# Optimization experiments

Measured on AMD Instinct MI355X. Metric: run time of the kernel, lower is better.

Reference implementation:

```python
import jax, jax.numpy as jnp
import numpy as np

B, N, DIN, A = 64, 64, 64, 32
DOUT = 128          # obs_output_dim == obs_act_output_dim == 128 (required by module wiring)
OA_IN = DIN + A     # obs_act_input_dim = 96


def _w(key, shape):
    fan_in = shape[-1]
    return jax.random.normal(key, shape, jnp.float32) / jnp.sqrt(jnp.float32(fan_in))


def setup_inputs() -> dict:
    key = jax.random.key(0)
    ks = jax.random.split(key, 14)
    return {
        "states": jax.random.normal(ks[0], (B, N, DIN), jnp.float32),
        "policies": jax.random.uniform(ks[1], (B, N, A), jnp.float32),
        "actions": jax.random.uniform(ks[2], (B, N, A), jnp.float32),
        # state_embed_preproc: Linear(obs_input_dim, 128) + LeakyReLU
        "W_se_pre": _w(ks[3], (128, DIN)),
        "b_se_pre": jnp.zeros((128,), jnp.float32),
        # key/query layers (shared between both attention stages in forward)
        "W_key": _w(ks[4], (DOUT, 128)),
        "W_query": _w(ks[5], (DOUT, 128)),
        # state_embed: Linear(obs_output_dim, 128) + LeakyReLU
        "W_se": _w(ks[6], (128, DOUT)),
        "b_se": jnp.zeros((128,), jnp.float32),
        # state_act_pol_embed: Linear(obs_act_input_dim, 128) + LeakyReLU
        "W_sap": _w(ks[7], (128, OA_IN)),
        "b_sap": jnp.zeros((128,), jnp.float32),
        # attention_value_layer: Linear(128, obs_act_output_dim)
        "W_av": _w(ks[8], (DOUT, 128)),
        # final value head
        "W_f1": _w(ks[9], (64, DOUT)),
        "W_f2": _w(ks[10], (1, 64)),
    }


def reference(states, policies, actions, W_se_pre, b_se_pre, W_key, W_query,
              W_se, b_se, W_sap, b_sap, W_av, W_f1, W_f2):
    lrelu = jax.nn.leaky_relu  # negative_slope=0.01, matches torch default
    d_k = W_key.shape[0]
    inv_sqrt_dk = 1.0 / jnp.sqrt(jnp.asarray(d_k, states.dtype))

    # stage 1: self-attention over agents on raw-state embeddings
    e = lrelu(states @ W_se_pre.T + b_se_pre)                       # [B,N,128]
    q1 = e @ W_query.T
    k1 = e @ W_key.T
    w_pre = jax.nn.softmax(jnp.einsum('bid,bjd->bij', q1, k1) * inv_sqrt_dk, axis=-1)
    # NB: attention_value_layer_preproc output is overwritten in the original forward;
    # the effective value is weight_preproc @ states_embed_preproc.
    av_pre = jnp.einsum('bij,bjd->bid', w_pre, e)                   # [B,N,128]

    # stage 2: self-attention weights over agents on re-embedded states
    se = lrelu(av_pre @ W_se.T + b_se)                              # [B,N,128]
    q2 = se @ W_query.T
    k2 = se @ W_key.T
    w = jax.nn.softmax(jnp.einsum('bid,bjd->bij', q2, k2) * inv_sqrt_dk, axis=-1)

    # obs_actions_policies[b,j,k] = (state_k, policy_k) if j==k else (state_k, action_k)
    obs_act = jnp.concatenate([states, actions], axis=-1)           # [B,N,OA_IN]
    obs_pol = jnp.concatenate([states, policies], axis=-1)
    n = states.shape[1]
    eye = jnp.eye(n, dtype=states.dtype)[None, :, :, None]          # [1,N,N,1]
    oap = eye * obs_pol[:, None, :, :] + (1.0 - eye) * obs_act[:, None, :, :]  # [B,N,N,OA_IN]

    emb = lrelu(oap @ W_sap.T + b_sap)                              # [B,N,N,128]
    av = emb @ W_av.T                                               # [B,N,N,DOUT]

    # fused form of repeat->weight->sum: node[b,i,j,d] = sum_k w[b,i,k] * av[b,j,k,d]
    node = jnp.einsum('bik,bjkd->bijd', w, av)                      # [B,N,N,DOUT]

    value = lrelu(node @ W_f1.T) @ W_f2.T                           # [B,N,N,1]
    return value, w_pre, w
```

## Files before the change

### kernel.cpp

```cpp
#include <hip/hip_runtime.h>

#define DEVFN __device__ __forceinline__

constexpr int BNN = 64 * 64 * 64;
constexpr float SCALE = 0.08838834764831845f;
constexpr float NSLOPE = 0.01f;

constexpr int OFF_WPRET = 0;
constexpr int OFF_WQT   = 8192;
constexpr int OFF_M     = 24576;
constexpr int OFF_WSET  = 40960;
constexpr int OFF_WSAPT = 57344;
constexpr int OFF_WAVT  = 69632;
constexpr int OFF_WF1T  = 86016;
constexpr int OFF_E     = 98304;
constexpr int OFF_Q     = 622592;
constexpr int OFF_ET    = 1146880;
constexpr int OFF_SET   = 1671168;
constexpr int OFF_AVACT = 2195456;
constexpr int OFF_HD    = 2719744;


DEVFN void st128(int tid, const float* __restrict__ src, float* __restrict__ Bs, int rows) {
  const int n4 = rows * 32;
  for (int idx = tid; idx < n4; idx += 512) {
    const int r = idx >> 5, c = idx & 31;
    *reinterpret_cast<float4*>(&Bs[r * 132 + c * 4]) =
        *reinterpret_cast<const float4*>(&src[r * 128 + c * 4]);
  }
}

DEVFN void st64x(int tid, const float* __restrict__ src, float* __restrict__ Bs) {
  for (int idx = tid; idx < 1024; idx += 512) {
    const int r = idx >> 4, c = idx & 15;
    *reinterpret_cast<float4*>(&Bs[r * 68 + c * 4]) =
        *reinterpret_cast<const float4*>(&src[r * 64 + c * 4]);
  }
}

DEVFN void wrT(int tid, const float* __restrict__ S, float* __restrict__ dst, int rq) {
  const int fr = tid >> 2, a4 = tid & 3;
  float t[4];
#pragma unroll
  for (int i = 0; i < 4; ++i) t[i] = S[(a4 * 4 + i) * 132 + fr];
  float4 v; v.x = t[0]; v.y = t[1]; v.z = t[2]; v.w = t[3];
  *reinterpret_cast<float4*>(&dst[fr * 64 + rq * 16 + a4 * 4]) = v;
}


DEVFN void g1(int tid, const float* __restrict__ A, int lda,
              const float* __restrict__ Bs, int K, float (&acc)[4]) {
  const int c0 = (tid & 31) * 4, rg = tid >> 5;
#pragma unroll 8
  for (int k = 0; k < K; ++k) {
    const float4 bv = *reinterpret_cast<const float4*>(&Bs[k * 132 + c0]);
    const float a = A[rg * lda + k];
    acc[0] += a * bv.x; acc[1] += a * bv.y; acc[2] += a * bv.z; acc[3] += a * bv.w;
  }
}

DEVFN void g2A(int tid, const float* __restrict__ A0, const float* __restrict__ A1,
               int lda, const float* __restrict__ Bs, int K,
               float (&a0)[4], float (&a1)[4]) {
  const int c0 = (tid & 31) * 4, rg = tid >> 5;
#pragma unroll 4
  for (int k = 0; k < K; ++k) {
    const float4 bv = *reinterpret_cast<const float4*>(&Bs[k * 132 + c0]);
    const float x = A0[rg * lda + k];
    const float y = A1[rg * lda + k];
    a0[0] += x * bv.x; a0[1] += x * bv.y; a0[2] += x * bv.z; a0[3] += x * bv.w;
    a1[0] += y * bv.x; a1[1] += y * bv.y; a1[2] += y * bv.z; a1[3] += y * bv.w;
  }
}

DEVFN void gH(int tid, const float* __restrict__ A, int lda,
              const float* __restrict__ Bs, int K, float (&acc)[2]) {
  const int c0 = (tid & 31) * 2, rg = tid >> 5;
#pragma unroll 8
  for (int k = 0; k < K; ++k) {
    const float2 bv = *reinterpret_cast<const float2*>(&Bs[k * 68 + c0]);
    const float a = A[rg * lda + k];
    acc[0] += a * bv.x; acc[1] += a * bv.y;
  }
}

template<bool ACT, bool HASB>
DEVFN void epi(int tid, const float (&acc)[4], float* __restrict__ O, int ldo,
               const float* __restrict__ bias) {
  const int c0 = (tid & 31) * 4, rg = tid >> 5;
  float t[4];
#pragma unroll
  for (int i = 0; i < 4; ++i) {
    float x = acc[i];
    if constexpr (HASB) x += bias[c0 + i];
    if constexpr (ACT) x = (x > 0.f) ? x : NSLOPE * x;
    t[i] = x;
  }
  float4 v; v.x = t[0]; v.y = t[1]; v.z = t[2]; v.w = t[3];
  *reinterpret_cast<float4*>(&O[rg * ldo + c0]) = v;
}


DEVFN void score_half(int tid, const float* __restrict__ Qs, int hoff,
                      const float* __restrict__ Ks, float (&acc)[2]) {
  const int j = tid & 63, iw = tid >> 6;
#pragma unroll 2
  for (int kt = 0; kt < 64; kt += 8) {
    float qv[2][8];
#pragma unroll
    for (int r = 0; r < 2; ++r) {
      *reinterpret_cast<float4*>(&qv[r][0]) =
          *reinterpret_cast<const float4*>(&Qs[(iw * 2 + r) * 132 + hoff + kt]);
      *reinterpret_cast<float4*>(&qv[r][4]) =
          *reinterpret_cast<const float4*>(&Qs[(iw * 2 + r) * 132 + hoff + kt + 4]);
    }
#pragma unroll
    for (int kk = 0; kk < 8; ++kk) {
      const float kv = Ks[(kt + kk) * 68 + j];
      acc[0] += qv[0][kk] * kv;
      acc[1] += qv[1][kk] * kv;
    }
  }
}

DEVFN void softmax_write(int tid, float (&acc)[2], float* __restrict__ Wp,
                         float* __restrict__ gout) {
  const int j = tid & 63, iw = tid >> 6;
#pragma unroll
  for (int r = 0; r < 2; ++r) {
    float v = acc[r] * SCALE;
    float m = v;
#pragma unroll
    for (int off = 32; off > 0; off >>= 1) m = fmaxf(m, __shfl_xor(m, off, 64));
    const float p = __expf(v - m);
    float s = p;
#pragma unroll
    for (int off = 32; off > 0; off >>= 1) s += __shfl_xor(s, off, 64);
    const float w = p / s;
    Wp[(iw * 2 + r) * 68 + j] = w;
    gout[(iw * 2 + r) * 64 + j] = w;
  }
}


__global__ void transpose_all(const float* __restrict__ Wpre, const float* __restrict__ Wq,
                              const float* __restrict__ Wse, const float* __restrict__ Wsap,
                              const float* __restrict__ Wav, const float* __restrict__ Wf1,
                              float* __restrict__ ws) {
  const int m = blockIdx.y;
  const float* src; int Cout, K, off;
  switch (m) {
    case 0: src = Wpre; Cout = 128; K = 64;  off = OFF_WPRET; break;
    case 1: src = Wq;   Cout = 128; K = 128; off = OFF_WQT;   break;
    case 2: src = Wse;  Cout = 128; K = 128; off = OFF_WSET;  break;
    case 3: src = Wsap; Cout = 128; K = 96;  off = OFF_WSAPT; break;
    case 4: src = Wav;  Cout = 128; K = 128; off = OFF_WAVT;  break;
    default: src = Wf1; Cout = 64;  K = 128; off = OFF_WF1T;  break;
  }
  const int idx = blockIdx.x * 256 + threadIdx.x;
  if (idx < Cout * K) {
    const int c = idx / K, k = idx - c * K;
    ws[off + k * Cout + c] = src[idx];
  }
}

__global__ __launch_bounds__(512) void make_M(const float* __restrict__ Wkey,
                                              float* __restrict__ ws) {
  __shared__ float As[16 * 132];
  __shared__ float Bs[64 * 132];
  const int tid = threadIdx.x;
  const int r0 = blockIdx.x * 16;
  {
    const int r = tid >> 5, c = tid & 31;
    *reinterpret_cast<float4*>(&As[r * 132 + c * 4]) =
        *reinterpret_cast<const float4*>(&ws[OFF_WQT + (r0 + r) * 128 + c * 4]);
  }
  const int c0 = (tid & 31) * 4, rg = tid >> 5;
  float acc[4] = {};
  for (int h = 0; h < 2; ++h) {
    __syncthreads();
    st128(tid, Wkey + h * 8192, Bs, 64);
    __syncthreads();
#pragma unroll 8
    for (int k = 0; k < 64; ++k) {
      const float4 bv = *reinterpret_cast<const float4*>(&Bs[k * 132 + c0]);
      const float a = As[rg * 132 + h * 64 + k];
      acc[0] += a * bv.x; acc[1] += a * bv.y; acc[2] += a * bv.z; acc[3] += a * bv.w;
    }
  }
  float4 v; v.x = acc[0]; v.y = acc[1]; v.z = acc[2]; v.w = acc[3];
  *reinterpret_cast<float4*>(&ws[OFF_M + (r0 + rg) * 128 + c0]) = v;
}

__global__ __launch_bounds__(512) void P1(const float* __restrict__ states,
                                          const float* __restrict__ policies,
                                          const float* __restrict__ actions,
                                          const float* __restrict__ b_sap,
                                          const float* __restrict__ b_se_pre,
                                          float* __restrict__ ws) {
  __shared__ float Xa[16 * 100], Xp[16 * 100];
  __shared__ float Ea[16 * 132], Ep[16 * 132], Dd[16 * 132], Er[16 * 132];
  __shared__ float Bs[64 * 132];
  const int tid = threadIdx.x;
  const int wid = ((blockIdx.x & 7) << 5) | (blockIdx.x >> 3);
  const int b = wid >> 2, rq = wid & 3;
  const int r0g = b * 64 + rq * 16;

  for (int idx = tid; idx < 1024; idx += 512) {
    const int r = idx >> 6, c = idx & 63;
    const float s = states[(r0g + r) * 64 + c];
    Xa[r * 100 + c] = s;
    Xp[r * 100 + c] = s;
  }
  {
    const int r = tid >> 5, c = tid & 31;
    Xa[r * 100 + 64 + c] = actions[(r0g + r) * 32 + c];
    Xp[r * 100 + 64 + c] = policies[(r0g + r) * 32 + c];
  }
  st128(tid, ws + OFF_WSAPT, Bs, 64);
  __syncthreads();
  float aa[4] = {}, ap[4] = {};
  g2A(tid, Xa, Xp, 100, Bs, 64, aa, ap);
  __syncthreads();
  st128(tid, ws + OFF_WSAPT + 8192, Bs, 32);
  __syncthreads();
  g2A(tid, Xa + 64, Xp + 64, 100, Bs, 32, aa, ap);
  epi<true, true>(tid, aa, Ea, 132, b_sap);
  epi<true, true>(tid, ap, Ep, 132, b_sap);
  __syncthreads();
  for (int idx = tid; idx < 2048; idx += 512) {
    const int r = idx >> 7, c = idx & 127;
    Ep[r * 132 + c] -= Ea[r * 132 + c];
  }
  __syncthreads();
  st128(tid, ws + OFF_WAVT, Bs, 64);
  __syncthreads();
  float av[4] = {}, dl[4] = {};
  g2A(tid, Ea, Ep, 132, Bs, 64, av, dl);
  __syncthreads();
  st128(tid, ws + OFF_WAVT + 8192, Bs, 64);
  __syncthreads();
  g2A(tid, Ea + 64, Ep + 64, 132, Bs, 64, av, dl);
  epi<false, false>(tid, av, ws + OFF_AVACT + r0g * 128, 128, nullptr);
  epi<false, false>(tid, dl, Dd, 132, nullptr);
  __syncthreads();
  st64x(tid, ws + OFF_WF1T, Bs);
  __syncthreads();
  float ah[2] = {};
  gH(tid, Dd, 132, Bs, 64, ah);
  __syncthreads();
  st64x(tid, ws + OFF_WF1T + 4096, Bs);
  __syncthreads();
  gH(tid, Dd + 64, 132, Bs, 64, ah);
  {
    const int c0 = (tid & 31) * 2, rg = tid >> 5;
    float2 v; v.x = ah[0]; v.y = ah[1];
    *reinterpret_cast<float2*>(&ws[OFF_HD + (r0g + rg) * 64 + c0]) = v;
  }
  __syncthreads();
  st128(tid, ws + OFF_WPRET, Bs, 64);
  __syncthreads();
  {
    float ae[4] = {};
    g1(tid, Xa, 100, Bs, 64, ae);
    const int c0 = (tid & 31) * 4, rg = tid >> 5;
    float t[4];
#pragma unroll
    for (int i = 0; i < 4; ++i) {
      float x = ae[i] + b_se_pre[c0 + i];
      t[i] = (x > 0.f) ? x : NSLOPE * x;
    }
    float4 v; v.x = t[0]; v.y = t[1]; v.z = t[2]; v.w = t[3];
    *reinterpret_cast<float4*>(&Er[rg * 132 + c0]) = v;
    *reinterpret_cast<float4*>(&ws[OFF_E + (r0g + rg) * 128 + c0]) = v;
  }
  __syncthreads();
  wrT(tid, Er, ws + OFF_ET + b * 8192, rq);
  st128(tid, ws + OFF_M, Bs, 64);
  __syncthreads();
  float af[4] = {};
  g1(tid, Er, 132, Bs, 64, af);
  __syncthreads();
  st128(tid, ws + OFF_M + 8192, Bs, 64);
  __syncthreads();
  g1(tid, Er + 64, 132, Bs, 64, af);
  epi<false, false>(tid, af, ws + OFF_Q + r0g * 128, 128, nullptr);
}

__global__ __launch_bounds__(512) void P3(const float* __restrict__ b_se,
                                          float* __restrict__ ws,
                                          float* __restrict__ out) {
  __shared__ float Qs[16 * 132];
  __shared__ float Bs[64 * 132];
  __shared__ float Wp[16 * 68], AV[16 * 132], SEr[16 * 132];
  const int tid = threadIdx.x;
  const int wid = ((blockIdx.x & 7) << 5) | (blockIdx.x >> 3);
  const int b = wid >> 2, rq = wid & 3;
  const int r0g = b * 64 + rq * 16;

  {
    const int r = tid >> 5, c = tid & 31;
    *reinterpret_cast<float4*>(&Qs[r * 132 + c * 4]) =
        *reinterpret_cast<const float4*>(&ws[OFF_Q + (r0g + r) * 128 + c * 4]);
  }
  st64x(tid, ws + OFF_ET + b * 8192, Bs);
  __syncthreads();
  float sc[2] = {};
  score_half(tid, Qs, 0, Bs, sc);
  __syncthreads();
  st64x(tid, ws + OFF_ET + b * 8192 + 4096, Bs);
  __syncthreads();
  score_half(tid, Qs, 64, Bs, sc);
  softmax_write(tid, sc, Wp, out + BNN + b * 4096 + rq * 1024);
  __syncthreads();
  st128(tid, ws + OFF_E + b * 8192, Bs, 64);
  __syncthreads();
  {
    float a[4] = {};
    g1(tid, Wp, 68, Bs, 64, a);
    epi<false, false>(tid, a, AV, 132, nullptr);
  }
  __syncthreads();
  st128(tid, ws + OFF_WSET, Bs, 64);
  __syncthreads();
  float as[4] = {};
  g1(tid, AV, 132, Bs, 64, as);
  __syncthreads();
  st128(tid, ws + OFF_WSET + 8192, Bs, 64);
  __syncthreads();
  g1(tid, AV + 64, 132, Bs, 64, as);
  {
    const int c0 = (tid & 31) * 4, rg = tid >> 5;
    float t[4];
#pragma unroll
    for (int i = 0; i < 4; ++i) {
      float x = as[i] + b_se[c0 + i];
      t[i] = (x > 0.f) ? x : NSLOPE * x;
    }
    float4 v; v.x = t[0]; v.y = t[1]; v.z = t[2]; v.w = t[3];
    *reinterpret_cast<float4*>(&SEr[rg * 132 + c0]) = v;
  }
  __syncthreads();
  wrT(tid, SEr, ws + OFF_SET + b * 8192, rq);
  st128(tid, ws + OFF_M, Bs, 64);
  __syncthreads();
  float af[4] = {};
  g1(tid, SEr, 132, Bs, 64, af);
  __syncthreads();
  st128(tid, ws + OFF_M + 8192, Bs, 64);
  __syncthreads();
  g1(tid, SEr + 64, 132, Bs, 64, af);
  epi<false, false>(tid, af, ws + OFF_Q + r0g * 128, 128, nullptr);
}

__global__ __launch_bounds__(512) void P4(const float* __restrict__ Wf2g,
                                          float* __restrict__ ws,
                                          float* __restrict__ out) {
  __shared__ float Qs[16 * 132];
  __shared__ float Bs[64 * 132];
  __shared__ float Wp[16 * 68], NB[16 * 132], Hb[16 * 66];
  __shared__ float Hd[64 * 69];
  __shared__ float Wf2s[64];
  const int tid = threadIdx.x;
  const int wid = ((blockIdx.x & 7) << 5) | (blockIdx.x >> 3);
  const int b = wid >> 2, rq = wid & 3;
  const int r0g = b * 64 + rq * 16;

  for (int idx = tid; idx < 4096; idx += 512)
    Hd[(idx >> 6) * 69 + (idx & 63)] = ws[OFF_HD + b * 4096 + idx];
  if (tid < 64) Wf2s[tid] = Wf2g[tid];
  {
    const int r = tid >> 5, c = tid & 31;
    *reinterpret_cast<float4*>(&Qs[r * 132 + c * 4]) =
        *reinterpret_cast<const float4*>(&ws[OFF_Q + (r0g + r) * 128 + c * 4]);
  }
  st64x(tid, ws + OFF_SET + b * 8192, Bs);
  __syncthreads();
  float sc[2] = {};
  score_half(tid, Qs, 0, Bs, sc);
  __syncthreads();
  st64x(tid, ws + OFF_SET + b * 8192 + 4096, Bs);
  __syncthreads();
  score_half(tid, Qs, 64, Bs, sc);
  softmax_write(tid, sc, Wp, out + 2 * BNN + b * 4096 + rq * 1024);
  __syncthreads();
  st128(tid, ws + OFF_AVACT + b * 8192, Bs, 64);
  __syncthreads();
  {
    float a[4] = {};
    g1(tid, Wp, 68, Bs, 64, a);
    epi<false, false>(tid, a, NB, 132, nullptr);
  }
  __syncthreads();
  st64x(tid, ws + OFF_WF1T, Bs);
  __syncthreads();
  float ah[2] = {};
  gH(tid, NB, 132, Bs, 64, ah);
  __syncthreads();
  st64x(tid, ws + OFF_WF1T + 4096, Bs);
  __syncthreads();
  gH(tid, NB + 64, 132, Bs, 64, ah);
  {
    const int c0 = (tid & 31) * 2, rg = tid >> 5;
    float2 v; v.x = ah[0]; v.y = ah[1];
    *reinterpret_cast<float2*>(&Hb[rg * 66 + c0]) = v;
  }
  __syncthreads();
  const int j = tid & 63, iw = tid >> 6;
  float wv[2], a2[2] = {0.f, 0.f};
#pragma unroll
  for (int r = 0; r < 2; ++r) wv[r] = Wp[(iw * 2 + r) * 68 + j];
  for (int f = 0; f < 64; ++f) {
    const float hdv = Hd[j * 69 + f];
    const float wf = Wf2s[f];
#pragma unroll
    for (int r = 0; r < 2; ++r) {
      float t = Hb[(iw * 2 + r) * 66 + f] + wv[r] * hdv;
      t = (t > 0.f) ? t : NSLOPE * t;
      a2[r] += t * wf;
    }
  }
#pragma unroll
  for (int r = 0; r < 2; ++r)
    out[(r0g + iw * 2 + r) * 64 + j] = a2[r];
}

extern "C" void kernel_launch(void* const* d_in, const int* in_sizes, int n_in,
                              void* d_out, int out_size, void* d_ws, size_t ws_size,
                              hipStream_t stream) {
  const float* states   = (const float*)d_in[0];
  const float* policies = (const float*)d_in[1];
  const float* actions  = (const float*)d_in[2];
  const float* W_se_pre = (const float*)d_in[3];
  const float* b_se_pre = (const float*)d_in[4];
  const float* W_key    = (const float*)d_in[5];
  const float* W_query  = (const float*)d_in[6];
  const float* W_se     = (const float*)d_in[7];
  const float* b_se     = (const float*)d_in[8];
  const float* W_sap    = (const float*)d_in[9];
  const float* b_sap    = (const float*)d_in[10];
  const float* W_av     = (const float*)d_in[11];
  const float* W_f1     = (const float*)d_in[12];
  const float* W_f2     = (const float*)d_in[13];
  float* out = (float*)d_out;
  float* ws  = (float*)d_ws;

  transpose_all<<<dim3(64, 6), dim3(256), 0, stream>>>(
      W_se_pre, W_query, W_se, W_sap, W_av, W_f1, ws);
  make_M<<<dim3(8), dim3(512), 0, stream>>>(W_key, ws);
  P1<<<dim3(256), dim3(512), 0, stream>>>(states, policies, actions, b_sap, b_se_pre, ws);
  P3<<<dim3(256), dim3(512), 0, stream>>>(b_se, ws, out);
  P4<<<dim3(256), dim3(512), 0, stream>>>(W_f2, ws, out);
}
```

Before: 68.45 us.

## Precompute av_act·Wf1 in P1 and share state projection across act/pol

P1 now computes the state part of the state-action-policy embedding once and adds separate action and policy contributions, instead of running the full 96-wide GEMM twice. It also multiplies the action-value rows by Wf1 up front, storing a 64-wide HA buffer in place of the 128-wide av_act. P4 can then apply the attention weights directly to HA (using linearity: (W·AV)·Wf1 = W·(AV·Wf1)), dropping a 64x128x64 GEMM and one set of Wf1 staging loads. This cuts P4 work and workspace traffic at the cost of a little extra GEMM work and one extra barrier in P1.

```diff
diff --git a/kernel.cpp b/kernel.cpp
--- a/kernel.cpp
+++ b/kernel.cpp
@@ -17,7 +17,7 @@
 constexpr int OFF_Q     = 622592;
 constexpr int OFF_ET    = 1146880;
 constexpr int OFF_SET   = 1671168;
-constexpr int OFF_AVACT = 2195456;
+constexpr int OFF_HA    = 2195456;
 constexpr int OFF_HD    = 2719744;
 
 
@@ -81,6 +81,20 @@
     const float2 bv = *reinterpret_cast<const float2*>(&Bs[k * 68 + c0]);
     const float a = A[rg * lda + k];
     acc[0] += a * bv.x; acc[1] += a * bv.y;
+  }
+}
+
+DEVFN void gH2(int tid, const float* __restrict__ A0, const float* __restrict__ A1,
+               int lda, const float* __restrict__ Bs, int K,
+               float (&a0)[2], float (&a1)[2]) {
+  const int c0 = (tid & 31) * 2, rg = tid >> 5;
+#pragma unroll 4
+  for (int k = 0; k < K; ++k) {
+    const float2 bv = *reinterpret_cast<const float2*>(&Bs[k * 68 + c0]);
+    const float x = A0[rg * lda + k];
+    const float y = A1[rg * lda + k];
+    a0[0] += x * bv.x; a0[1] += x * bv.y;
+    a1[0] += y * bv.x; a1[1] += y * bv.y;
   }
 }
 
@@ -198,8 +212,10 @@
                                           const float* __restrict__ b_sap,
                                           const float* __restrict__ b_se_pre,
                                           float* __restrict__ ws) {
-  __shared__ float Xa[16 * 100], Xp[16 * 100];
-  __shared__ float Ea[16 * 132], Ep[16 * 132], Dd[16 * 132], Er[16 * 132];
+  __shared__ float S[16 * 68];
+  __shared__ float Aa[16 * 36], Ap[16 * 36];
+  __shared__ float Ea[16 * 132];
+  __shared__ float Ep[16 * 132], Dd[16 * 132], Er[16 * 132];
   __shared__ float Bs[64 * 132];
   const int tid = threadIdx.x;
   const int wid = ((blockIdx.x & 7) << 5) | (blockIdx.x >> 3);
@@ -208,23 +224,23 @@
 
   for (int idx = tid; idx < 1024; idx += 512) {
     const int r = idx >> 6, c = idx & 63;
-    const float s = states[(r0g + r) * 64 + c];
-    Xa[r * 100 + c] = s;
-    Xp[r * 100 + c] = s;
+    S[r * 68 + c] = states[(r0g + r) * 64 + c];
   }
   {
     const int r = tid >> 5, c = tid & 31;
-    Xa[r * 100 + 64 + c] = actions[(r0g + r) * 32 + c];
-    Xp[r * 100 + 64 + c] = policies[(r0g + r) * 32 + c];
+    Aa[r * 36 + c] = actions[(r0g + r) * 32 + c];
+    Ap[r * 36 + c] = policies[(r0g + r) * 32 + c];
   }
   st128(tid, ws + OFF_WSAPT, Bs, 64);
   __syncthreads();
-  float aa[4] = {}, ap[4] = {};
-  g2A(tid, Xa, Xp, 100, Bs, 64, aa, ap);
+  float cm[4] = {};
+  g1(tid, S, 68, Bs, 64, cm);
   __syncthreads();
   st128(tid, ws + OFF_WSAPT + 8192, Bs, 32);
   __syncthreads();
-  g2A(tid, Xa + 64, Xp + 64, 100, Bs, 32, aa, ap);
+  float aa[4] = {cm[0], cm[1], cm[2], cm[3]};
+  float ap[4] = {cm[0], cm[1], cm[2], cm[3]};
+  g2A(tid, Aa, Ap, 36, Bs, 32, aa, ap);
   epi<true, true>(tid, aa, Ea, 132, b_sap);
   epi<true, true>(tid, ap, Ep, 132, b_sap);
   __syncthreads();
@@ -241,28 +257,31 @@
   st128(tid, ws + OFF_WAVT + 8192, Bs, 64);
   __syncthreads();
   g2A(tid, Ea + 64, Ep + 64, 132, Bs, 64, av, dl);
-  epi<false, false>(tid, av, ws + OFF_AVACT + r0g * 128, 128, nullptr);
+  __syncthreads();
+  epi<false, false>(tid, av, Ea, 132, nullptr);
   epi<false, false>(tid, dl, Dd, 132, nullptr);
   __syncthreads();
   st64x(tid, ws + OFF_WF1T, Bs);
   __syncthreads();
-  float ah[2] = {};
-  gH(tid, Dd, 132, Bs, 64, ah);
+  float ah[2] = {}, aha[2] = {};
+  gH2(tid, Dd, Ea, 132, Bs, 64, ah, aha);
   __syncthreads();
   st64x(tid, ws + OFF_WF1T + 4096, Bs);
   __syncthreads();
-  gH(tid, Dd + 64, 132, Bs, 64, ah);
+  gH2(tid, Dd + 64, Ea + 64, 132, Bs, 64, ah, aha);
   {
     const int c0 = (tid & 31) * 2, rg = tid >> 5;
-    float2 v; v.x = ah[0]; v.y = ah[1];
-    *reinterpret_cast<float2*>(&ws[OFF_HD + (r0g + rg) * 64 + c0]) = v;
+    float2 vh; vh.x = ah[0]; vh.y = ah[1];
+    float2 va; va.x = aha[0]; va.y = aha[1];
+    *reinterpret_cast<float2*>(&ws[OFF_HD + (r0g + rg) * 64 + c0]) = vh;
+    *reinterpret_cast<float2*>(&ws[OFF_HA + (r0g + rg) * 64 + c0]) = va;
   }
   __syncthreads();
   st128(tid, ws + OFF_WPRET, Bs, 64);
   __syncthreads();
   {
     float ae[4] = {};
-    g1(tid, Xa, 100, Bs, 64, ae);
+    g1(tid, S, 68, Bs, 64, ae);
     const int c0 = (tid & 31) * 4, rg = tid >> 5;
     float t[4];
 #pragma unroll
@@ -358,7 +377,7 @@
                                           float* __restrict__ out) {
   __shared__ float Qs[16 * 132];
   __shared__ float Bs[64 * 132];
-  __shared__ float Wp[16 * 68], NB[16 * 132], Hb[16 * 66];
+  __shared__ float Wp[16 * 68], Hb[16 * 66];
   __shared__ float Hd[64 * 69];
   __shared__ float Wf2s[64];
   const int tid = threadIdx.x;
@@ -384,22 +403,10 @@
   score_half(tid, Qs, 64, Bs, sc);
   softmax_write(tid, sc, Wp, out + 2 * BNN + b * 4096 + rq * 1024);
   __syncthreads();
-  st128(tid, ws + OFF_AVACT + b * 8192, Bs, 64);
-  __syncthreads();
-  {
-    float a[4] = {};
-    g1(tid, Wp, 68, Bs, 64, a);
-    epi<false, false>(tid, a, NB, 132, nullptr);
-  }
-  __syncthreads();
-  st64x(tid, ws + OFF_WF1T, Bs);
+  st64x(tid, ws + OFF_HA + b * 4096, Bs);
   __syncthreads();
   float ah[2] = {};
-  gH(tid, NB, 132, Bs, 64, ah);
-  __syncthreads();
-  st64x(tid, ws + OFF_WF1T + 4096, Bs);
-  __syncthreads();
-  gH(tid, NB + 64, 132, Bs, 64, ah);
+  gH(tid, Wp, 68, Bs, 64, ah);
   {
     const int c0 = (tid & 31) * 2, rg = tid >> 5;
     float2 v; v.x = ah[0]; v.y = ah[1];
```

Result: faster. 64.59 us (-5.6%).
